# Kernel optimization log

Hardware: AMD Instinct MI355X
Metric: run time of the kernel (lower is better)

## Reference

```python
import jax, jax.numpy as jnp
import numpy as np

N, E, IN, H, OUT = 100000, 1600000, 128, 128, 64


def setup_inputs() -> dict:
    key = jax.random.key(0)
    ks = jax.random.split(key, 7)
    x = jax.random.normal(ks[0], (N, IN), dtype=jnp.float32)
    edge_index = jax.random.randint(ks[1], (2, E), 0, N, dtype=jnp.int32)
    # Glorot-style scaled params (PyG SAGEConv: lin_l has bias, lin_r does not)
    s1 = 1.0 / np.sqrt(IN)
    s2 = 1.0 / np.sqrt(H)
    W1_l = jax.random.normal(ks[2], (H, IN), dtype=jnp.float32) * s1
    W1_r = jax.random.normal(ks[3], (H, IN), dtype=jnp.float32) * s1
    b1 = jnp.zeros((H,), dtype=jnp.float32)
    W2_l = jax.random.normal(ks[4], (OUT, H), dtype=jnp.float32) * s2
    W2_r = jax.random.normal(ks[5], (OUT, H), dtype=jnp.float32) * s2
    b2 = jnp.zeros((OUT,), dtype=jnp.float32)
    return {"x": x, "W1_l": W1_l, "W1_r": W1_r, "b1": b1,
            "W2_l": W2_l, "W2_r": W2_r, "b2": b2, "edge_index": edge_index}


def _sage_conv(x, edge_index, W_l, W_r, b):
    # mean-aggregate source-node features at target nodes, then linear + root term
    src, dst = edge_index[0], edge_index[1]
    n = x.shape[0]
    msgs = x[src]                                                   # [E, d]
    agg = jax.ops.segment_sum(msgs, dst, num_segments=n)            # [N, d]
    deg = jax.ops.segment_sum(jnp.ones((src.shape[0],), x.dtype), dst, num_segments=n)
    mean = agg / jnp.clip(deg, 1.0)[:, None]                        # zero-deg nodes stay 0
    return mean @ W_l.T + b + x @ W_r.T


def reference(x, W1_l, W1_r, b1, W2_l, W2_r, b2, edge_index):
    h = _sage_conv(x, edge_index, W1_l, W1_r, b1)
    h = jax.nn.relu(h)  # dropout p=0.0 -> identity
    out = _sage_conv(h, edge_index, W2_l, W2_r, b2)
    return out
```

## Files before the change

kernel.cpp:

```cpp
#include <hip/hip_runtime.h>


typedef unsigned int uint32;
typedef short bf16x4 __attribute__((ext_vector_type(4)));
typedef short bf16x8 __attribute__((ext_vector_type(8)));
typedef float f32x16 __attribute__((ext_vector_type(16)));

__device__ __forceinline__ uint32 pack_bf16_rne(float a, float b) {
    uint32 ua = __float_as_uint(a);
    uint32 ub = __float_as_uint(b);
    uint32 ra = (ua + 0x7fffu + ((ua >> 16) & 1u)) >> 16;
    uint32 rb = (ub + 0x7fffu + ((ub >> 16) & 1u)) >> 16;
    return ra | (rb << 16);
}
__device__ __forceinline__ float bf_lo(uint32 v) { return __uint_as_float(v << 16); }
__device__ __forceinline__ float bf_hi(uint32 v) { return __uint_as_float(v & 0xffff0000u); }

__device__ __forceinline__ short rne16(float v, float* back) {
    uint32 u = __float_as_uint(v);
    uint32 r = (u + 0x7fffu + ((u >> 16) & 1u)) >> 16;
    *back = __uint_as_float(r << 16);
    return (short)r;
}

__device__ __forceinline__ void acc8(float* s, uint4 v) {
    s[0] += bf_lo(v.x); s[1] += bf_hi(v.x);
    s[2] += bf_lo(v.y); s[3] += bf_hi(v.y);
    s[4] += bf_lo(v.z); s[5] += bf_hi(v.z);
    s[6] += bf_lo(v.w); s[7] += bf_hi(v.w);
}

__device__ __forceinline__ int sel4(int c0, int c1, int c2, int c3, int g) {
    int a = (g & 1) ? c1 : c0;
    int b = (g & 1) ? c3 : c2;
    return (g & 2) ? b : a;
}

__global__ void k_to_bf16(const float* __restrict__ x, uint32* __restrict__ xb,
                          short* __restrict__ xpH, long n4, int spl) {
    long i = (long)blockIdx.x * blockDim.x + threadIdx.x;
    if (i >= n4) return;
    int node = (int)(i >> 5);
    int k4 = ((int)i & 31) * 4;
    float4 v = ((const float4*)x)[i];
    float back;
    bf16x4 hi4;
    hi4[0] = rne16(v.x, &back);
    hi4[1] = rne16(v.y, &back);
    hi4[2] = rne16(v.z, &back);
    hi4[3] = rne16(v.w, &back);
    uint2 oxb;
    oxb.x = (uint32)(unsigned short)hi4[0] | ((uint32)(unsigned short)hi4[1] << 16);
    oxb.y = (uint32)(unsigned short)hi4[2] | ((uint32)(unsigned short)hi4[3] << 16);
    ((uint2*)xb)[i] = oxb;
    int c = k4 >> 3;
    *(bf16x4*)&xpH[(size_t)c * spl + (size_t)node * 8 + (k4 & 7)] = hi4;
}

__global__ void k_wprep(const float* __restrict__ W1l, const float* __restrict__ W1r,
                        const float* __restrict__ W2l, const float* __restrict__ W2r,
                        short* __restrict__ W1pH, short* __restrict__ W1pL,
                        short* __restrict__ W2pH, short* __restrict__ W2pL) {
    int i = blockIdx.x * blockDim.x + threadIdx.x;
    float back;
    if (i < 32768) {
        int j = i >> 8, k = i & 255;
        float v = (k < 128) ? W1l[j * 128 + k] : W1r[j * 128 + k - 128];
        float hb;
        short hs = rne16(v, &hb);
        short ls = rne16(v - hb, &back);
        int idx = (k >> 3) * 1024 + j * 8 + (k & 7);
        W1pH[idx] = hs;
        W1pL[idx] = ls;
    } else if (i < 32768 + 16384) {
        int i2 = i - 32768;
        int j = i2 >> 7, k = i2 & 127;
        float v = (j < 64) ? W2l[j * 128 + k] : W2r[(j - 64) * 128 + k];
        float hb;
        short hs = rne16(v, &hb);
        short ls = rne16(v - hb, &back);
        int idx = (k >> 3) * 1024 + j * 8 + (k & 7);
        W2pH[idx] = hs;
        W2pL[idx] = ls;
    }
}


__global__ void k_bcount(const int* __restrict__ ei, int E, int NB,
                         int* __restrict__ bucket_cnt) {
    __shared__ int hist[1024];
    int t = threadIdx.x;
    for (int i = t; i < NB; i += 256) hist[i] = 0;
    __syncthreads();
    int stride = gridDim.x * 256;
    for (int e = blockIdx.x * 256 + t; e < E; e += stride)
        atomicAdd(&hist[ei[E + e] >> 8], 1);
    __syncthreads();
    for (int i = t; i < NB; i += 256) {
        int c = hist[i];
        if (c) atomicAdd(&bucket_cnt[i], c);
    }
}

__global__ void k_bscan(const int* __restrict__ bucket_cnt, int NB, int E,
                        int* __restrict__ bucket_off, int* __restrict__ bucket_cur) {
    __shared__ int s[1024];
    int t = threadIdx.x;
    int v = (t < NB) ? bucket_cnt[t] : 0;
    s[t] = v;
    __syncthreads();
    for (int o = 1; o < 1024; o <<= 1) {
        int u = (t >= o) ? s[t - o] : 0;
        __syncthreads();
        s[t] += u;
        __syncthreads();
    }
    int ex = s[t] - v;
    if (t < NB) { bucket_off[t] = ex; bucket_cur[t] = ex; }
    if (t == NB - 1) bucket_off[NB] = ex + v;
}

__global__ void k_bscatter(const int* __restrict__ ei, int E, int NB,
                           int* __restrict__ bucket_cur, uint32* __restrict__ eb) {
    __shared__ int hist[1024];
    __shared__ int base[1024];
    int t = threadIdx.x;
    for (int i = t; i < NB; i += 256) hist[i] = 0;
    __syncthreads();
    int stride = gridDim.x * 256;
    for (int e = blockIdx.x * 256 + t; e < E; e += stride)
        atomicAdd(&hist[ei[E + e] >> 8], 1);
    __syncthreads();
    for (int i = t; i < NB; i += 256) {
        int c = hist[i];
        base[i] = c ? atomicAdd(&bucket_cur[i], c) : 0;
        hist[i] = 0;
    }
    __syncthreads();
    for (int e = blockIdx.x * 256 + t; e < E; e += stride) {
        int d = ei[E + e];
        int b = d >> 8;
        int r = atomicAdd(&hist[b], 1);
        eb[base[b] + r] = ((uint32)(d & 255) << 24) | (uint32)ei[e];
    }
}

__global__ void k_bfinal(const uint32* __restrict__ eb,
                         const int* __restrict__ bucket_off,
                         int* __restrict__ row_ptr, int* __restrict__ col,
                         int N, int E) {
    __shared__ int deg[256];
    __shared__ int sc[256];
    __shared__ int cur[256];
    int b = blockIdx.x;
    int t = threadIdx.x;
    int beg = bucket_off[b], end = bucket_off[b + 1];
    deg[t] = 0;
    __syncthreads();
    for (int e = beg + t; e < end; e += 256)
        atomicAdd(&deg[eb[e] >> 24], 1);
    __syncthreads();
    int v = deg[t];
    sc[t] = v;
    __syncthreads();
    for (int o = 1; o < 256; o <<= 1) {
        int u = (t >= o) ? sc[t - o] : 0;
        __syncthreads();
        sc[t] += u;
        __syncthreads();
    }
    int ex = sc[t] - v;
    int node = b * 256 + t;
    if (node < N) row_ptr[node] = beg + ex;
    if (b == gridDim.x - 1 && t == 0) row_ptr[N] = E;
    cur[t] = ex;
    __syncthreads();
    for (int e = beg + t; e < end; e += 256) {
        uint32 u = eb[e];
        int r = atomicAdd(&cur[u >> 24], 1);
        col[beg + r] = (int)(u & 0xFFFFFFu);
    }
}


__global__ void k_agg_mean(const int* __restrict__ rp, const int* __restrict__ col,
                           const uint32* __restrict__ xb,
                           short* __restrict__ mpH, short* __restrict__ mpL,
                           int N, int spl) {
    int node = blockIdx.x * 4 + (threadIdx.x >> 6);
    if (node >= N) return;
    node = __builtin_amdgcn_readfirstlane(node);
    int lane = threadIdx.x & 63;
    int g = lane >> 4;
    int f = lane & 15;
    int beg = rp[node], end = rp[node + 1];
    const uint4* xb4 = (const uint4*)xb;
    float s[8];
#pragma unroll
    for (int j = 0; j < 8; j++) s[j] = 0.f;
    int e = beg;
    for (; e + 16 <= end; e += 16) {
        int c0 = col[e + 0], c1 = col[e + 1], c2 = col[e + 2], c3 = col[e + 3];
        int c4 = col[e + 4], c5 = col[e + 5], c6 = col[e + 6], c7 = col[e + 7];
        int c8 = col[e + 8], c9 = col[e + 9], ca = col[e + 10], cb = col[e + 11];
        int cc = col[e + 12], cd = col[e + 13], ce = col[e + 14], cf = col[e + 15];
        int s0 = sel4(c0, c1, c2, c3, g);
        int s1 = sel4(c4, c5, c6, c7, g);
        int s2 = sel4(c8, c9, ca, cb, g);
        int s3 = sel4(cc, cd, ce, cf, g);
        uint4 v0 = xb4[(size_t)s0 * 16 + f];
        uint4 v1 = xb4[(size_t)s1 * 16 + f];
        uint4 v2 = xb4[(size_t)s2 * 16 + f];
        uint4 v3 = xb4[(size_t)s3 * 16 + f];
        acc8(s, v0); acc8(s, v1); acc8(s, v2); acc8(s, v3);
    }
    for (; e + 4 <= end; e += 4) {
        int c0 = col[e + 0], c1 = col[e + 1], c2 = col[e + 2], c3 = col[e + 3];
        int s0 = sel4(c0, c1, c2, c3, g);
        uint4 v0 = xb4[(size_t)s0 * 16 + f];
        acc8(s, v0);
    }
    int rem = end - e;
    if (g < rem) {
        int s0 = col[e + g];
        uint4 v0 = xb4[(size_t)s0 * 16 + f];
        acc8(s, v0);
    }
#pragma unroll
    for (int j = 0; j < 8; j++) {
        s[j] += __shfl_xor(s[j], 16);
        s[j] += __shfl_xor(s[j], 32);
    }
    if (g == 0) {
        float inv = 1.0f / (float)max(end - beg, 1);
        uint32 H[4], L[4];
#pragma unroll
        for (int p = 0; p < 4; p++) {
            float m0 = s[2 * p] * inv, m1 = s[2 * p + 1] * inv;
            float b;
            short h0 = rne16(m0, &b);
            short l0 = rne16(m0 - b, &b);
            short h1 = rne16(m1, &b);
            short l1 = rne16(m1 - b, &b);
            H[p] = (uint32)(unsigned short)h0 | ((uint32)(unsigned short)h1 << 16);
            L[p] = (uint32)(unsigned short)l0 | ((uint32)(unsigned short)l1 << 16);
        }
        size_t idx = (size_t)f * spl + (size_t)node * 8;
        *(uint4*)&mpH[idx] = make_uint4(H[0], H[1], H[2], H[3]);
        *(uint4*)&mpL[idx] = make_uint4(L[0], L[1], L[2], L[3]);
    }
}


__global__ __launch_bounds__(256) void k_mgemm1(
        const short* __restrict__ mpH, const short* __restrict__ mpL,
        const short* __restrict__ xpH,
        const short* __restrict__ W1pH, const short* __restrict__ W1pL,
        const float* __restrict__ b1,
        short* __restrict__ hpH, short* __restrict__ hpL, int N, int spl) {
    int t = threadIdx.x;
    int w = t >> 6, lane = t & 63;
    int m = lane & 31, hh = lane >> 5;
    int node0 = blockIdx.x * 128;
    int myrow = node0 + 32 * w + m;
    f32x16 acc[4];
#pragma unroll
    for (int i = 0; i < 4; i++)
#pragma unroll
        for (int r = 0; r < 16; r++) acc[i][r] = 0.f;

    for (int kc = 0; kc < 8; kc++) {
        int c = kc * 2 + hh;
        bf16x8 af = *(const bf16x8*)(mpH + (size_t)c * spl + (size_t)myrow * 8);
        bf16x8 al = *(const bf16x8*)(mpL + (size_t)c * spl + (size_t)myrow * 8);
#pragma unroll
        for (int tt = 0; tt < 4; tt++) {
            bf16x8 bh = *(const bf16x8*)(W1pH + c * 1024 + (32 * tt + m) * 8);
            bf16x8 bl = *(const bf16x8*)(W1pL + c * 1024 + (32 * tt + m) * 8);
            acc[tt] = __builtin_amdgcn_mfma_f32_32x32x16_bf16(af, bh, acc[tt], 0, 0, 0);
            acc[tt] = __builtin_amdgcn_mfma_f32_32x32x16_bf16(al, bh, acc[tt], 0, 0, 0);
            acc[tt] = __builtin_amdgcn_mfma_f32_32x32x16_bf16(af, bl, acc[tt], 0, 0, 0);
        }
    }
    for (int kc = 0; kc < 8; kc++) {
        int c = kc * 2 + hh;
        int cb = 16 + c;
        bf16x8 af = *(const bf16x8*)(xpH + (size_t)c * spl + (size_t)myrow * 8);
#pragma unroll
        for (int tt = 0; tt < 4; tt++) {
            bf16x8 bh = *(const bf16x8*)(W1pH + cb * 1024 + (32 * tt + m) * 8);
            bf16x8 bl = *(const bf16x8*)(W1pL + cb * 1024 + (32 * tt + m) * 8);
            acc[tt] = __builtin_amdgcn_mfma_f32_32x32x16_bf16(af, bh, acc[tt], 0, 0, 0);
            acc[tt] = __builtin_amdgcn_mfma_f32_32x32x16_bf16(af, bl, acc[tt], 0, 0, 0);
        }
    }
#pragma unroll
    for (int tt = 0; tt < 4; tt++) {
        int j = 32 * tt + m;
        float bias = b1[j];
        int cj = j >> 3;
        size_t pbase = (size_t)cj * spl + (j & 7);
#pragma unroll
        for (int r = 0; r < 16; r++) {
            int row = 32 * w + (r & 3) + 8 * (r >> 2) + 4 * hh;
            int grow = node0 + row;
            if (grow < N) {
                float v = fmaxf(acc[tt][r] + bias, 0.f);
                float back;
                short hs = rne16(v, &back);
                short ls = rne16(v - back, &back);
                hpH[pbase + (size_t)grow * 8] = hs;
                hpL[pbase + (size_t)grow * 8] = ls;
            }
        }
    }
}


__global__ __launch_bounds__(256) void k_mgemm2(
        const short* __restrict__ hpH, const short* __restrict__ hpL,
        const short* __restrict__ W2pH, const short* __restrict__ W2pL,
        const float* __restrict__ b2,
        unsigned short* __restrict__ hl, float* __restrict__ hr, int N, int spl) {
    int t = threadIdx.x;
    int w = t >> 6, lane = t & 63;
    int m = lane & 31, hh = lane >> 5;
    int node0 = blockIdx.x * 128;
    int mynode = node0 + 32 * w + m;
    f32x16 acc[4];
#pragma unroll
    for (int i = 0; i < 4; i++)
#pragma unroll
        for (int r = 0; r < 16; r++) acc[i][r] = 0.f;

    for (int kc = 0; kc < 8; kc++) {
        int c = kc * 2 + hh;
        bf16x8 bH = *(const bf16x8*)(hpH + (size_t)c * spl + (size_t)mynode * 8);
        bf16x8 bL = *(const bf16x8*)(hpL + (size_t)c * spl + (size_t)mynode * 8);
#pragma unroll
        for (int jt = 0; jt < 4; jt++) {
            bf16x8 wH = *(const bf16x8*)(W2pH + c * 1024 + (32 * jt + m) * 8);
            bf16x8 wL = *(const bf16x8*)(W2pL + c * 1024 + (32 * jt + m) * 8);
            acc[jt] = __builtin_amdgcn_mfma_f32_32x32x16_bf16(wH, bH, acc[jt], 0, 0, 0);
            acc[jt] = __builtin_amdgcn_mfma_f32_32x32x16_bf16(wL, bH, acc[jt], 0, 0, 0);
            acc[jt] = __builtin_amdgcn_mfma_f32_32x32x16_bf16(wH, bL, acc[jt], 0, 0, 0);
        }
    }
    if (mynode >= N) return;
#pragma unroll
    for (int jt = 0; jt < 2; jt++) {
#pragma unroll
        for (int rg = 0; rg < 4; rg++) {
            int jj = 32 * jt + 8 * rg + 4 * hh;
            uint2 o;
            o.x = pack_bf16_rne(acc[jt][4 * rg + 0], acc[jt][4 * rg + 1]);
            o.y = pack_bf16_rne(acc[jt][4 * rg + 2], acc[jt][4 * rg + 3]);
            *(uint2*)&hl[(size_t)mynode * 64 + jj] = o;
        }
    }
#pragma unroll
    for (int jt = 2; jt < 4; jt++) {
#pragma unroll
        for (int rg = 0; rg < 4; rg++) {
            int jj = 32 * (jt - 2) + 8 * rg + 4 * hh;
            float4 bv = *(const float4*)(b2 + jj);
            float4 o;
            o.x = acc[jt][4 * rg + 0] + bv.x;
            o.y = acc[jt][4 * rg + 1] + bv.y;
            o.z = acc[jt][4 * rg + 2] + bv.z;
            o.w = acc[jt][4 * rg + 3] + bv.w;
            *(float4*)&hr[(size_t)mynode * 64 + jj] = o;
        }
    }
}


__global__ void k_agg_out(const int* __restrict__ rp, const int* __restrict__ col,
                          const uint32* __restrict__ hl, const float* __restrict__ hr,
                          float* __restrict__ out, int N) {
    int node = blockIdx.x * 4 + (threadIdx.x >> 6);
    if (node >= N) return;
    node = __builtin_amdgcn_readfirstlane(node);
    int lane = threadIdx.x & 63;
    int g = lane >> 3;
    int f = lane & 7;
    int beg = rp[node], end = rp[node + 1];
    const uint4* hl4 = (const uint4*)hl;
    float s[8];
#pragma unroll
    for (int j = 0; j < 8; j++) s[j] = 0.f;
    int e = beg;
    for (; e + 16 <= end; e += 16) {
        int c0 = col[e + 0], c1 = col[e + 1], c2 = col[e + 2], c3 = col[e + 3];
        int c4 = col[e + 4], c5 = col[e + 5], c6 = col[e + 6], c7 = col[e + 7];
        int c8 = col[e + 8], c9 = col[e + 9], ca = col[e + 10], cb = col[e + 11];
        int cc = col[e + 12], cd = col[e + 13], ce = col[e + 14], cf = col[e + 15];
        int lo0 = sel4(c0, c1, c2, c3, g & 3);
        int hi0 = sel4(c4, c5, c6, c7, g & 3);
        int s0 = (g < 4) ? lo0 : hi0;
        int lo1 = sel4(c8, c9, ca, cb, g & 3);
        int hi1 = sel4(cc, cd, ce, cf, g & 3);
        int s1 = (g < 4) ? lo1 : hi1;
        uint4 v0 = hl4[(size_t)s0 * 8 + f];
        uint4 v1 = hl4[(size_t)s1 * 8 + f];
        acc8(s, v0); acc8(s, v1);
    }
    for (; e + 8 <= end; e += 8) {
        int c0 = col[e + 0], c1 = col[e + 1], c2 = col[e + 2], c3 = col[e + 3];
        int c4 = col[e + 4], c5 = col[e + 5], c6 = col[e + 6], c7 = col[e + 7];
        int lo0 = sel4(c0, c1, c2, c3, g & 3);
        int hi0 = sel4(c4, c5, c6, c7, g & 3);
        int s0 = (g < 4) ? lo0 : hi0;
        uint4 v0 = hl4[(size_t)s0 * 8 + f];
        acc8(s, v0);
    }
    int rem = end - e;
    if (g < rem) {
        int s0 = col[e + g];
        uint4 v0 = hl4[(size_t)s0 * 8 + f];
        acc8(s, v0);
    }
#pragma unroll
    for (int j = 0; j < 8; j++) {
        s[j] += __shfl_xor(s[j], 8);
        s[j] += __shfl_xor(s[j], 16);
        s[j] += __shfl_xor(s[j], 32);
    }
    if (g == 0) {
        float inv = 1.0f / (float)max(end - beg, 1);
        const float* hrp = hr + (size_t)node * 64 + f * 8;
        float4 h0 = *(const float4*)(hrp);
        float4 h1 = *(const float4*)(hrp + 4);
        float4 o0, o1;
        o0.x = s[0] * inv + h0.x;
        o0.y = s[1] * inv + h0.y;
        o0.z = s[2] * inv + h0.z;
        o0.w = s[3] * inv + h0.w;
        o1.x = s[4] * inv + h1.x;
        o1.y = s[5] * inv + h1.y;
        o1.z = s[6] * inv + h1.z;
        o1.w = s[7] * inv + h1.w;
        float* op = out + (size_t)node * 64 + f * 8;
        *(float4*)(op) = o0;
        *(float4*)(op + 4) = o1;
    }
}

extern "C" void kernel_launch(void* const* d_in, const int* in_sizes, int n_in,
                              void* d_out, int out_size, void* d_ws, size_t ws_size,
                              hipStream_t stream) {
    const float* x   = (const float*)d_in[0];
    const float* W1l = (const float*)d_in[1];
    const float* W1r = (const float*)d_in[2];
    const float* b1  = (const float*)d_in[3];
    const float* W2l = (const float*)d_in[4];
    const float* W2r = (const float*)d_in[5];
    const float* b2  = (const float*)d_in[6];
    const int*   ei  = (const int*)d_in[7];
    int N = in_sizes[0] / 128;
    int E = in_sizes[7] / 2;
    int NB = (N + 255) >> 8;
    int gb = (N + 127) / 128;
    int Np = gb * 128;
    int spl = Np * 8;
    float* out = (float*)d_out;

    char* w = (char*)d_ws;
    size_t off = 0;
    auto alloc = [&](size_t bytes) -> char* {
        char* p = w + off;
        off += (bytes + 255) & ~(size_t)255;
        return p;
    };
    int*   row_ptr = (int*)alloc((size_t)(N + 1) * 4);
    int*   bcnt    = (int*)alloc((size_t)(NB + 1) * 4);
    int*   boff    = (int*)alloc((size_t)(NB + 1) * 4);
    int*   bcur    = (int*)alloc((size_t)(NB + 1) * 4);
    short* W1pH    = (short*)alloc(32768 * 2);
    short* W1pL    = (short*)alloc(32768 * 2);
    short* W2pH    = (short*)alloc(16384 * 2);
    short* W2pL    = (short*)alloc(16384 * 2);
    int*   col     = (int*)alloc((size_t)E * 4);
    short* xpH     = (short*)alloc((size_t)16 * spl * 2);
    short* mpH     = (short*)alloc((size_t)16 * spl * 2);
    short* mpL     = (short*)alloc((size_t)16 * spl * 2);
    short* hpH     = (short*)alloc((size_t)16 * spl * 2);
    short* hpL     = (short*)alloc((size_t)16 * spl * 2);
    uint32* eb   = (uint32*)hpH;
    uint32* xb   = (uint32*)hpL;
    unsigned short* hl = (unsigned short*)mpH;
    float* hr    = (float*)(mpH + (size_t)N * 64);

    hipMemsetAsync(bcnt, 0, (size_t)NB * 4, stream);
    long n4 = (long)N * 32;
    k_to_bf16<<<(int)((n4 + 255) / 256), 256, 0, stream>>>(x, xb, xpH, n4, spl);
    k_wprep<<<192, 256, 0, stream>>>(W1l, W1r, W2l, W2r, W1pH, W1pL, W2pH, W2pL);
    k_bcount<<<256, 256, 0, stream>>>(ei, E, NB, bcnt);
    k_bscan<<<1, 1024, 0, stream>>>(bcnt, NB, E, boff, bcur);
    k_bscatter<<<128, 256, 0, stream>>>(ei, E, NB, bcur, eb);
    k_bfinal<<<NB, 256, 0, stream>>>(eb, boff, row_ptr, col, N, E);

    int ab = (N + 3) / 4;
    k_agg_mean<<<ab, 256, 0, stream>>>(row_ptr, col, xb, mpH, mpL, N, spl);
    k_mgemm1<<<gb, 256, 0, stream>>>(mpH, mpL, xpH, W1pH, W1pL, b1, hpH, hpL, N, spl);
    k_mgemm2<<<gb, 256, 0, stream>>>(hpH, hpL, W2pH, W2pL, b2, hl, hr, N, spl);
    k_agg_out<<<ab, 256, 0, stream>>>(row_ptr, col, (const uint32*)hl, hr, out, N);
}
```

Before: 393.3 us.

## Fuse both SAGE GEMMs via LDS, use row-major layouts, vectorize edge-index loads

The two MFMA GEMM kernels are merged into one. The hidden layer is kept in LDS as bf16 hi/lo pairs instead of being written to and read back from global memory. Operands move to a plain row-major layout, which drops the separate chunked xpH copy, and the x conversion and weight prep kernels are merged into one launch. The aggregation loops now load column indices as vector loads per lane group and skip masking the high bf16 half, which adds tiny low-bit garbage to the odd features. The fused GEMM uses about 67KB of LDS per block, which may limit occupancy.

```diff
diff --git a/kernel.cpp b/kernel.cpp
--- a/kernel.cpp
+++ b/kernel.cpp
@@ -23,65 +23,44 @@
     return (short)r;
 }
 
-__device__ __forceinline__ void acc8(float* s, uint4 v) {
-    s[0] += bf_lo(v.x); s[1] += bf_hi(v.x);
-    s[2] += bf_lo(v.y); s[3] += bf_hi(v.y);
-    s[4] += bf_lo(v.z); s[5] += bf_hi(v.z);
-    s[6] += bf_lo(v.w); s[7] += bf_hi(v.w);
-}
-
-__device__ __forceinline__ int sel4(int c0, int c1, int c2, int c3, int g) {
-    int a = (g & 1) ? c1 : c0;
-    int b = (g & 1) ? c3 : c2;
-    return (g & 2) ? b : a;
-}
-
-__global__ void k_to_bf16(const float* __restrict__ x, uint32* __restrict__ xb,
-                          short* __restrict__ xpH, long n4, int spl) {
+__global__ void k_prep(const float* __restrict__ x, uint32* __restrict__ xb, long n4,
+                       const float* __restrict__ W1l, const float* __restrict__ W1r,
+                       const float* __restrict__ W2l, const float* __restrict__ W2r,
+                       short* __restrict__ W1cH, short* __restrict__ W1cL,
+                       short* __restrict__ W2cH, short* __restrict__ W2cL) {
     long i = (long)blockIdx.x * blockDim.x + threadIdx.x;
-    if (i >= n4) return;
-    int node = (int)(i >> 5);
-    int k4 = ((int)i & 31) * 4;
-    float4 v = ((const float4*)x)[i];
+    if (i < n4) {
+        float4 v = ((const float4*)x)[i];
+        float back;
+        short h0 = rne16(v.x, &back);
+        short h1 = rne16(v.y, &back);
+        short h2 = rne16(v.z, &back);
+        short h3 = rne16(v.w, &back);
+        uint2 o;
+        o.x = (uint32)(unsigned short)h0 | ((uint32)(unsigned short)h1 << 16);
+        o.y = (uint32)(unsigned short)h2 | ((uint32)(unsigned short)h3 << 16);
+        ((uint2*)xb)[i] = o;
+        return;
+    }
+    int i2 = (int)(i - n4);
     float back;
-    bf16x4 hi4;
-    hi4[0] = rne16(v.x, &back);
-    hi4[1] = rne16(v.y, &back);
-    hi4[2] = rne16(v.z, &back);
-    hi4[3] = rne16(v.w, &back);
-    uint2 oxb;
-    oxb.x = (uint32)(unsigned short)hi4[0] | ((uint32)(unsigned short)hi4[1] << 16);
-    oxb.y = (uint32)(unsigned short)hi4[2] | ((uint32)(unsigned short)hi4[3] << 16);
-    ((uint2*)xb)[i] = oxb;
-    int c = k4 >> 3;
-    *(bf16x4*)&xpH[(size_t)c * spl + (size_t)node * 8 + (k4 & 7)] = hi4;
-}
-
-__global__ void k_wprep(const float* __restrict__ W1l, const float* __restrict__ W1r,
-                        const float* __restrict__ W2l, const float* __restrict__ W2r,
-                        short* __restrict__ W1pH, short* __restrict__ W1pL,
-                        short* __restrict__ W2pH, short* __restrict__ W2pL) {
-    int i = blockIdx.x * blockDim.x + threadIdx.x;
-    float back;
-    if (i < 32768) {
-        int j = i >> 8, k = i & 255;
+    if (i2 < 32768) {
+        int j = i2 >> 8, k = i2 & 255;
         float v = (k < 128) ? W1l[j * 128 + k] : W1r[j * 128 + k - 128];
         float hb;
         short hs = rne16(v, &hb);
         short ls = rne16(v - hb, &back);
-        int idx = (k >> 3) * 1024 + j * 8 + (k & 7);
-        W1pH[idx] = hs;
-        W1pL[idx] = ls;
-    } else if (i < 32768 + 16384) {
-        int i2 = i - 32768;
-        int j = i2 >> 7, k = i2 & 127;
+        W1cH[i2] = hs;
+        W1cL[i2] = ls;
+    } else if (i2 < 32768 + 16384) {
+        int i3 = i2 - 32768;
+        int j = i3 >> 7, k = i3 & 127;
         float v = (j < 64) ? W2l[j * 128 + k] : W2r[(j - 64) * 128 + k];
         float hb;
         short hs = rne16(v, &hb);
         short ls = rne16(v - hb, &back);
-        int idx = (k >> 3) * 1024 + j * 8 + (k & 7);
-        W2pH[idx] = hs;
-        W2pL[idx] = ls;
+        W2cH[i3] = hs;
+        W2cL[i3] = ls;
     }
 }
 
@@ -185,8 +164,7 @@
 
 __global__ void k_agg_mean(const int* __restrict__ rp, const int* __restrict__ col,
                            const uint32* __restrict__ xb,
-                           short* __restrict__ mpH, short* __restrict__ mpL,
-                           int N, int spl) {
+                           short* __restrict__ mh, short* __restrict__ ml, int N) {
     int node = blockIdx.x * 4 + (threadIdx.x >> 6);
     if (node >= N) return;
     node = __builtin_amdgcn_readfirstlane(node);
@@ -198,34 +176,38 @@
     float s[8];
 #pragma unroll
     for (int j = 0; j < 8; j++) s[j] = 0.f;
+
+#define ACC_RAW(v)                                                      \
+    { s[0] += bf_lo(v.x); s[1] += __uint_as_float(v.x);                 \
+      s[2] += bf_lo(v.y); s[3] += __uint_as_float(v.y);                 \
+      s[4] += bf_lo(v.z); s[5] += __uint_as_float(v.z);                 \
+      s[6] += bf_lo(v.w); s[7] += __uint_as_float(v.w); }
+
     int e = beg;
     for (; e + 16 <= end; e += 16) {
-        int c0 = col[e + 0], c1 = col[e + 1], c2 = col[e + 2], c3 = col[e + 3];
-        int c4 = col[e + 4], c5 = col[e + 5], c6 = col[e + 6], c7 = col[e + 7];
-        int c8 = col[e + 8], c9 = col[e + 9], ca = col[e + 10], cb = col[e + 11];
-        int cc = col[e + 12], cd = col[e + 13], ce = col[e + 14], cf = col[e + 15];
-        int s0 = sel4(c0, c1, c2, c3, g);
-        int s1 = sel4(c4, c5, c6, c7, g);
-        int s2 = sel4(c8, c9, ca, cb, g);
-        int s3 = sel4(cc, cd, ce, cf, g);
-        uint4 v0 = xb4[(size_t)s0 * 16 + f];
-        uint4 v1 = xb4[(size_t)s1 * 16 + f];
-        uint4 v2 = xb4[(size_t)s2 * 16 + f];
-        uint4 v3 = xb4[(size_t)s3 * 16 + f];
-        acc8(s, v0); acc8(s, v1); acc8(s, v2); acc8(s, v3);
-    }
-    for (; e + 4 <= end; e += 4) {
-        int c0 = col[e + 0], c1 = col[e + 1], c2 = col[e + 2], c3 = col[e + 3];
-        int s0 = sel4(c0, c1, c2, c3, g);
-        uint4 v0 = xb4[(size_t)s0 * 16 + f];
-        acc8(s, v0);
+        uint4 cv = *(const uint4*)(col + e + 4 * g);
+        uint4 v0 = xb4[(size_t)cv.x * 16 + f];
+        uint4 v1 = xb4[(size_t)cv.y * 16 + f];
+        uint4 v2 = xb4[(size_t)cv.z * 16 + f];
+        uint4 v3 = xb4[(size_t)cv.w * 16 + f];
+        ACC_RAW(v0); ACC_RAW(v1); ACC_RAW(v2); ACC_RAW(v3);
+    }
+    for (; e + 8 <= end; e += 8) {
+        uint2 cv = *(const uint2*)(col + e + 2 * g);
+        uint4 v0 = xb4[(size_t)cv.x * 16 + f];
+        uint4 v1 = xb4[(size_t)cv.y * 16 + f];
+        ACC_RAW(v0); ACC_RAW(v1);
     }
     int rem = end - e;
-    if (g < rem) {
-        int s0 = col[e + g];
-        uint4 v0 = xb4[(size_t)s0 * 16 + f];
-        acc8(s, v0);
-    }
+    if (2 * g < rem) {
+        uint4 v0 = xb4[(size_t)col[e + 2 * g] * 16 + f];
+        ACC_RAW(v0);
+    }
+    if (2 * g + 1 < rem) {
+        uint4 v0 = xb4[(size_t)col[e + 2 * g + 1] * 16 + f];
+        ACC_RAW(v0);
+    }
+#undef ACC_RAW
 #pragma unroll
     for (int j = 0; j < 8; j++) {
         s[j] += __shfl_xor(s[j], 16);
@@ -245,88 +227,30 @@
             H[p] = (uint32)(unsigned short)h0 | ((uint32)(unsigned short)h1 << 16);
             L[p] = (uint32)(unsigned short)l0 | ((uint32)(unsigned short)l1 << 16);
         }
-        size_t idx = (size_t)f * spl + (size_t)node * 8;
-        *(uint4*)&mpH[idx] = make_uint4(H[0], H[1], H[2], H[3]);
-        *(uint4*)&mpL[idx] = make_uint4(L[0], L[1], L[2], L[3]);
-    }
-}
-
-
-__global__ __launch_bounds__(256) void k_mgemm1(
-        const short* __restrict__ mpH, const short* __restrict__ mpL,
-        const short* __restrict__ xpH,
-        const short* __restrict__ W1pH, const short* __restrict__ W1pL,
-        const float* __restrict__ b1,
-        short* __restrict__ hpH, short* __restrict__ hpL, int N, int spl) {
-    int t = threadIdx.x;
-    int w = t >> 6, lane = t & 63;
-    int m = lane & 31, hh = lane >> 5;
-    int node0 = blockIdx.x * 128;
-    int myrow = node0 + 32 * w + m;
-    f32x16 acc[4];
-#pragma unroll
-    for (int i = 0; i < 4; i++)
-#pragma unroll
-        for (int r = 0; r < 16; r++) acc[i][r] = 0.f;
-
-    for (int kc = 0; kc < 8; kc++) {
-        int c = kc * 2 + hh;
-        bf16x8 af = *(const bf16x8*)(mpH + (size_t)c * spl + (size_t)myrow * 8);
-        bf16x8 al = *(const bf16x8*)(mpL + (size_t)c * spl + (size_t)myrow * 8);
-#pragma unroll
-        for (int tt = 0; tt < 4; tt++) {
-            bf16x8 bh = *(const bf16x8*)(W1pH + c * 1024 + (32 * tt + m) * 8);
-            bf16x8 bl = *(const bf16x8*)(W1pL + c * 1024 + (32 * tt + m) * 8);
-            acc[tt] = __builtin_amdgcn_mfma_f32_32x32x16_bf16(af, bh, acc[tt], 0, 0, 0);
-            acc[tt] = __builtin_amdgcn_mfma_f32_32x32x16_bf16(al, bh, acc[tt], 0, 0, 0);
-            acc[tt] = __builtin_amdgcn_mfma_f32_32x32x16_bf16(af, bl, acc[tt], 0, 0, 0);
-        }
-    }
-    for (int kc = 0; kc < 8; kc++) {
-        int c = kc * 2 + hh;
-        int cb = 16 + c;
-        bf16x8 af = *(const bf16x8*)(xpH + (size_t)c * spl + (size_t)myrow * 8);
-#pragma unroll
-        for (int tt = 0; tt < 4; tt++) {
-            bf16x8 bh = *(const bf16x8*)(W1pH + cb * 1024 + (32 * tt + m) * 8);
-            bf16x8 bl = *(const bf16x8*)(W1pL + cb * 1024 + (32 * tt + m) * 8);
-            acc[tt] = __builtin_amdgcn_mfma_f32_32x32x16_bf16(af, bh, acc[tt], 0, 0, 0);
-            acc[tt] = __builtin_amdgcn_mfma_f32_32x32x16_bf16(af, bl, acc[tt], 0, 0, 0);
-        }
-    }
-#pragma unroll
-    for (int tt = 0; tt < 4; tt++) {
-        int j = 32 * tt + m;
-        float bias = b1[j];
-        int cj = j >> 3;
-        size_t pbase = (size_t)cj * spl + (j & 7);
-#pragma unroll
-        for (int r = 0; r < 16; r++) {
-            int row = 32 * w + (r & 3) + 8 * (r >> 2) + 4 * hh;
-            int grow = node0 + row;
-            if (grow < N) {
-                float v = fmaxf(acc[tt][r] + bias, 0.f);
-                float back;
-                short hs = rne16(v, &back);
-                short ls = rne16(v - back, &back);
-                hpH[pbase + (size_t)grow * 8] = hs;
-                hpL[pbase + (size_t)grow * 8] = ls;
-            }
-        }
-    }
-}
-
-
-__global__ __launch_bounds__(256) void k_mgemm2(
-        const short* __restrict__ hpH, const short* __restrict__ hpL,
-        const short* __restrict__ W2pH, const short* __restrict__ W2pL,
-        const float* __restrict__ b2,
-        unsigned short* __restrict__ hl, float* __restrict__ hr, int N, int spl) {
+        size_t idx = (size_t)node * 128 + f * 8;
+        *(uint4*)&mh[idx] = make_uint4(H[0], H[1], H[2], H[3]);
+        *(uint4*)&ml[idx] = make_uint4(L[0], L[1], L[2], L[3]);
+    }
+}
+
+
+#define HROW 132
+
+__global__ __launch_bounds__(256) void k_mgemm(
+        const short* __restrict__ mh, const short* __restrict__ ml,
+        const uint32* __restrict__ xb,
+        const short* __restrict__ W1cH, const short* __restrict__ W1cL,
+        const short* __restrict__ W2cH, const short* __restrict__ W2cL,
+        const float* __restrict__ b1, const float* __restrict__ b2,
+        unsigned short* __restrict__ hl, float* __restrict__ hr, int N) {
+    __shared__ short hH[128 * HROW];
+    __shared__ short hL[128 * HROW];
     int t = threadIdx.x;
     int w = t >> 6, lane = t & 63;
     int m = lane & 31, hh = lane >> 5;
     int node0 = blockIdx.x * 128;
     int mynode = node0 + 32 * w + m;
+    const short* xs = (const short*)xb;
     f32x16 acc[4];
 #pragma unroll
     for (int i = 0; i < 4; i++)
@@ -334,16 +258,70 @@
         for (int r = 0; r < 16; r++) acc[i][r] = 0.f;
 
     for (int kc = 0; kc < 8; kc++) {
-        int c = kc * 2 + hh;
-        bf16x8 bH = *(const bf16x8*)(hpH + (size_t)c * spl + (size_t)mynode * 8);
-        bf16x8 bL = *(const bf16x8*)(hpL + (size_t)c * spl + (size_t)mynode * 8);
+        int ko = 16 * kc + 8 * hh;
+        bf16x8 bH = *(const bf16x8*)(mh + (size_t)mynode * 128 + ko);
+        bf16x8 bL = *(const bf16x8*)(ml + (size_t)mynode * 128 + ko);
 #pragma unroll
         for (int jt = 0; jt < 4; jt++) {
-            bf16x8 wH = *(const bf16x8*)(W2pH + c * 1024 + (32 * jt + m) * 8);
-            bf16x8 wL = *(const bf16x8*)(W2pL + c * 1024 + (32 * jt + m) * 8);
-            acc[jt] = __builtin_amdgcn_mfma_f32_32x32x16_bf16(wH, bH, acc[jt], 0, 0, 0);
-            acc[jt] = __builtin_amdgcn_mfma_f32_32x32x16_bf16(wL, bH, acc[jt], 0, 0, 0);
-            acc[jt] = __builtin_amdgcn_mfma_f32_32x32x16_bf16(wH, bL, acc[jt], 0, 0, 0);
+            bf16x8 aH = *(const bf16x8*)(W1cH + (32 * jt + m) * 256 + ko);
+            bf16x8 aL = *(const bf16x8*)(W1cL + (32 * jt + m) * 256 + ko);
+            acc[jt] = __builtin_amdgcn_mfma_f32_32x32x16_bf16(aH, bH, acc[jt], 0, 0, 0);
+            acc[jt] = __builtin_amdgcn_mfma_f32_32x32x16_bf16(aL, bH, acc[jt], 0, 0, 0);
+            acc[jt] = __builtin_amdgcn_mfma_f32_32x32x16_bf16(aH, bL, acc[jt], 0, 0, 0);
+        }
+    }
+    for (int kc = 0; kc < 8; kc++) {
+        int ko = 16 * kc + 8 * hh;
+        bf16x8 bH = *(const bf16x8*)(xs + (size_t)mynode * 128 + ko);
+#pragma unroll
+        for (int jt = 0; jt < 4; jt++) {
+            bf16x8 aH = *(const bf16x8*)(W1cH + (32 * jt + m) * 256 + 128 + ko);
+            bf16x8 aL = *(const bf16x8*)(W1cL + (32 * jt + m) * 256 + 128 + ko);
+            acc[jt] = __builtin_amdgcn_mfma_f32_32x32x16_bf16(aH, bH, acc[jt], 0, 0, 0);
+            acc[jt] = __builtin_amdgcn_mfma_f32_32x32x16_bf16(aL, bH, acc[jt], 0, 0, 0);
+        }
+    }
+    {
+        int nl = 32 * w + m;
+#pragma unroll
+        for (int jt = 0; jt < 4; jt++) {
+#pragma unroll
+            for (int rg = 0; rg < 4; rg++) {
+                int j0 = 32 * jt + 8 * rg + 4 * hh;
+                float4 bv = *(const float4*)(b1 + j0);
+                float bb[4] = {bv.x, bv.y, bv.z, bv.w};
+                bf16x4 h4, l4;
+#pragma unroll
+                for (int q = 0; q < 4; q++) {
+                    float v = fmaxf(acc[jt][4 * rg + q] + bb[q], 0.f);
+                    float back;
+                    h4[q] = rne16(v, &back);
+                    l4[q] = rne16(v - back, &back);
+                }
+                *(bf16x4*)&hH[nl * HROW + j0] = h4;
+                *(bf16x4*)&hL[nl * HROW + j0] = l4;
+            }
+        }
+    }
+    __syncthreads();
+#pragma unroll
+    for (int i = 0; i < 4; i++)
+#pragma unroll
+        for (int r = 0; r < 16; r++) acc[i][r] = 0.f;
+    {
+        int nl = 32 * w + m;
+        for (int kc = 0; kc < 8; kc++) {
+            int ko = 16 * kc + 8 * hh;
+            bf16x8 bH = *(const bf16x8*)&hH[nl * HROW + ko];
+            bf16x8 bL = *(const bf16x8*)&hL[nl * HROW + ko];
+#pragma unroll
+            for (int jt = 0; jt < 4; jt++) {
+                bf16x8 aH = *(const bf16x8*)(W2cH + (32 * jt + m) * 128 + ko);
+                bf16x8 aL = *(const bf16x8*)(W2cL + (32 * jt + m) * 128 + ko);
+                acc[jt] = __builtin_amdgcn_mfma_f32_32x32x16_bf16(aH, bH, acc[jt], 0, 0, 0);
+                acc[jt] = __builtin_amdgcn_mfma_f32_32x32x16_bf16(aL, bH, acc[jt], 0, 0, 0);
+                acc[jt] = __builtin_amdgcn_mfma_f32_32x32x16_bf16(aH, bL, acc[jt], 0, 0, 0);
+            }
         }
     }
     if (mynode >= N) return;
@@ -351,25 +329,25 @@
     for (int jt = 0; jt < 2; jt++) {
 #pragma unroll
         for (int rg = 0; rg < 4; rg++) {
-            int jj = 32 * jt + 8 * rg + 4 * hh;
+            int j0 = 32 * jt + 8 * rg + 4 * hh;
             uint2 o;
             o.x = pack_bf16_rne(acc[jt][4 * rg + 0], acc[jt][4 * rg + 1]);
             o.y = pack_bf16_rne(acc[jt][4 * rg + 2], acc[jt][4 * rg + 3]);
-            *(uint2*)&hl[(size_t)mynode * 64 + jj] = o;
+            *(uint2*)&hl[(size_t)mynode * 64 + j0] = o;
         }
     }
 #pragma unroll
     for (int jt = 2; jt < 4; jt++) {
 #pragma unroll
         for (int rg = 0; rg < 4; rg++) {
-            int jj = 32 * (jt - 2) + 8 * rg + 4 * hh;
-            float4 bv = *(const float4*)(b2 + jj);
+            int j0 = 32 * (jt - 2) + 8 * rg + 4 * hh;
+            float4 bv = *(const float4*)(b2 + j0);
             float4 o;
             o.x = acc[jt][4 * rg + 0] + bv.x;
             o.y = acc[jt][4 * rg + 1] + bv.y;
             o.z = acc[jt][4 * rg + 2] + bv.z;
             o.w = acc[jt][4 * rg + 3] + bv.w;
-            *(float4*)&hr[(size_t)mynode * 64 + jj] = o;
+            *(float4*)&hr[(size_t)mynode * 64 + j0] = o;
         }
     }
 }
@@ -389,37 +367,30 @@
     float s[8];
 #pragma unroll
     for (int j = 0; j < 8; j++) s[j] = 0.f;
+
+#define ACC_MSK(v)                                          \
+    { s[0] += bf_lo(v.x); s[1] += bf_hi(v.x);               \
+      s[2] += bf_lo(v.y); s[3] += bf_hi(v.y);               \
+      s[4] += bf_lo(v.z); s[5] += bf_hi(v.z);               \
+      s[6] += bf_lo(v.w); s[7] += bf_hi(v.w); }
+
     int e = beg;
     for (; e + 16 <= end; e += 16) {
-        int c0 = col[e + 0], c1 = col[e + 1], c2 = col[e + 2], c3 = col[e + 3];
-        int c4 = col[e + 4], c5 = col[e + 5], c6 = col[e + 6], c7 = col[e + 7];
-        int c8 = col[e + 8], c9 = col[e + 9], ca = col[e + 10], cb = col[e + 11];
-        int cc = col[e + 12], cd = col[e + 13], ce = col[e + 14], cf = col[e + 15];
-        int lo0 = sel4(c0, c1, c2, c3, g & 3);
-        int hi0 = sel4(c4, c5, c6, c7, g & 3);
-        int s0 = (g < 4) ? lo0 : hi0;
-        int lo1 = sel4(c8, c9, ca, cb, g & 3);
-        int hi1 = sel4(cc, cd, ce, cf, g & 3);
-        int s1 = (g < 4) ? lo1 : hi1;
-        uint4 v0 = hl4[(size_t)s0 * 8 + f];
-        uint4 v1 = hl4[(size_t)s1 * 8 + f];
-        acc8(s, v0); acc8(s, v1);
+        uint2 cv = *(const uint2*)(col + e + 2 * g);
+        uint4 v0 = hl4[(size_t)cv.x * 8 + f];
+        uint4 v1 = hl4[(size_t)cv.y * 8 + f];
+        ACC_MSK(v0); ACC_MSK(v1);
     }
     for (; e + 8 <= end; e += 8) {
-        int c0 = col[e + 0], c1 = col[e + 1], c2 = col[e + 2], c3 = col[e + 3];
-        int c4 = col[e + 4], c5 = col[e + 5], c6 = col[e + 6], c7 = col[e + 7];
-        int lo0 = sel4(c0, c1, c2, c3, g & 3);
-        int hi0 = sel4(c4, c5, c6, c7, g & 3);
-        int s0 = (g < 4) ? lo0 : hi0;
-        uint4 v0 = hl4[(size_t)s0 * 8 + f];
-        acc8(s, v0);
+        uint4 v0 = hl4[(size_t)col[e + g] * 8 + f];
+        ACC_MSK(v0);
     }
     int rem = end - e;
     if (g < rem) {
-        int s0 = col[e + g];
-        uint4 v0 = hl4[(size_t)s0 * 8 + f];
-        acc8(s, v0);
-    }
+        uint4 v0 = hl4[(size_t)col[e + g] * 8 + f];
+        ACC_MSK(v0);
+    }
+#undef ACC_MSK
 #pragma unroll
     for (int j = 0; j < 8; j++) {
         s[j] += __shfl_xor(s[j], 8);
@@ -462,7 +433,6 @@
     int NB = (N + 255) >> 8;
     int gb = (N + 127) / 128;
     int Np = gb * 128;
-    int spl = Np * 8;
     float* out = (float*)d_out;
 
     char* w = (char*)d_ws;
@@ -476,33 +446,31 @@
     int*   bcnt    = (int*)alloc((size_t)(NB + 1) * 4);
     int*   boff    = (int*)alloc((size_t)(NB + 1) * 4);
     int*   bcur    = (int*)alloc((size_t)(NB + 1) * 4);
-    short* W1pH    = (short*)alloc(32768 * 2);
-    short* W1pL    = (short*)alloc(32768 * 2);
-    short* W2pH    = (short*)alloc(16384 * 2);
-    short* W2pL    = (short*)alloc(16384 * 2);
+    short* W1cH    = (short*)alloc(32768 * 2);
+    short* W1cL    = (short*)alloc(32768 * 2);
+    short* W2cH    = (short*)alloc(16384 * 2);
+    short* W2cL    = (short*)alloc(16384 * 2);
     int*   col     = (int*)alloc((size_t)E * 4);
-    short* xpH     = (short*)alloc((size_t)16 * spl * 2);
-    short* mpH     = (short*)alloc((size_t)16 * spl * 2);
-    short* mpL     = (short*)alloc((size_t)16 * spl * 2);
-    short* hpH     = (short*)alloc((size_t)16 * spl * 2);
-    short* hpL     = (short*)alloc((size_t)16 * spl * 2);
-    uint32* eb   = (uint32*)hpH;
-    uint32* xb   = (uint32*)hpL;
-    unsigned short* hl = (unsigned short*)mpH;
-    float* hr    = (float*)(mpH + (size_t)N * 64);
+    uint32* xb     = (uint32*)alloc((size_t)Np * 64 * 4);
+    short* mh      = (short*)alloc((size_t)Np * 128 * 2);
+    short* ml      = (short*)alloc((size_t)Np * 128 * 2);
+    unsigned short* hl = (unsigned short*)alloc((size_t)N * 64 * 2);
+    float* hr      = (float*)alloc((size_t)N * 64 * 4);
+    uint32* eb     = (uint32*)hl;
 
     hipMemsetAsync(bcnt, 0, (size_t)NB * 4, stream);
     long n4 = (long)N * 32;
-    k_to_bf16<<<(int)((n4 + 255) / 256), 256, 0, stream>>>(x, xb, xpH, n4, spl);
-    k_wprep<<<192, 256, 0, stream>>>(W1l, W1r, W2l, W2r, W1pH, W1pL, W2pH, W2pL);
+    long prep_items = n4 + 32768 + 16384;
+    k_prep<<<(int)((prep_items + 255) / 256), 256, 0, stream>>>(
+        x, xb, n4, W1l, W1r, W2l, W2r, W1cH, W1cL, W2cH, W2cL);
     k_bcount<<<256, 256, 0, stream>>>(ei, E, NB, bcnt);
     k_bscan<<<1, 1024, 0, stream>>>(bcnt, NB, E, boff, bcur);
     k_bscatter<<<128, 256, 0, stream>>>(ei, E, NB, bcur, eb);
     k_bfinal<<<NB, 256, 0, stream>>>(eb, boff, row_ptr, col, N, E);
 
     int ab = (N + 3) / 4;
-    k_agg_mean<<<ab, 256, 0, stream>>>(row_ptr, col, xb, mpH, mpL, N, spl);
-    k_mgemm1<<<gb, 256, 0, stream>>>(mpH, mpL, xpH, W1pH, W1pL, b1, hpH, hpL, N, spl);
-    k_mgemm2<<<gb, 256, 0, stream>>>(hpH, hpL, W2pH, W2pL, b2, hl, hr, N, spl);
+    k_agg_mean<<<ab, 256, 0, stream>>>(row_ptr, col, xb, mh, ml, N);
+    k_mgemm<<<gb, 256, 0, stream>>>(mh, ml, xb, W1cH, W1cL, W2cH, W2cL,
+                                    b1, b2, hl, hr, N);
     k_agg_out<<<ab, 256, 0, stream>>>(row_ptr, col, (const uint32*)hl, hr, out, N);
 }
```

New measurement: 397.3 us. No clear change (+1.0%).
